# Performance work log

Measured on AMD Instinct MI355X. Metric: run time of the kernel, lower is better.

## Reference

```python
import jax, jax.numpy as jnp
import numpy as np

N_TOKEN = 100000
D = 1024  # d_embed == d_model == d_proj
CUTOFFS = [0, 20000, 60000, 100000]  # cutoff_ends
N_SEQ = 2048


def setup_inputs() -> dict:
    key = jax.random.key(0)
    ks = jax.random.split(key, 20)
    w = lambda k, s: jax.random.normal(k, s, dtype=jnp.float32) * 0.02
    return {
        "x": jax.random.randint(ks[0], (N_SEQ,), 0, N_TOKEN),
        "labels": jax.random.randint(ks[1], (N_SEQ,), 0, N_TOKEN),
        # adaptive embedding tables (d_emb_i = 1024 / 4**i) and projections [d_proj, d_emb_i]
        "emb_w0": w(ks[2], (20000, 1024)),
        "emb_w1": w(ks[3], (40000, 256)),
        "emb_w2": w(ks[4], (40000, 64)),
        "emb_proj0": w(ks[5], (1024, 1024)),
        "emb_proj1": w(ks[6], (1024, 256)),
        "emb_proj2": w(ks[7], (1024, 64)),
        # adaptive softmax output layers + projections
        "out_w0": w(ks[8], (20000, 1024)),
        "out_b0": jnp.zeros((20000,), jnp.float32),
        "out_w1": w(ks[9], (40000, 256)),
        "out_b1": jnp.zeros((40000,), jnp.float32),
        "out_w2": w(ks[10], (40000, 64)),
        "out_b2": jnp.zeros((40000,), jnp.float32),
        "out_proj0": w(ks[11], (1024, 1024)),
        "out_proj1": w(ks[12], (1024, 256)),
        "out_proj2": w(ks[13], (1024, 64)),
        # cluster head tokens (one per tail cluster)
        "cluster_w": w(ks[14], (2, 1024)),
        "cluster_b": jnp.zeros((2,), jnp.float32),
    }


def _forward(x, labels,
             emb_w0, emb_w1, emb_w2, emb_proj0, emb_proj1, emb_proj2,
             out_w0, out_b0, out_w1, out_b1, out_w2, out_b2,
             out_proj0, out_proj1, out_proj2, cluster_w, cluster_b):
    scale = jnp.asarray(D ** 0.5, jnp.float32)
    # AdaptiveEmbedding (div_val>1): per-cluster embed -> project to d_proj, scatter by range.
    # Equivalent vectorized form: build the full projected table once, then gather.
    table = jnp.concatenate([
        emb_w0 @ emb_proj0.T,   # [20000, D]
        emb_w1 @ emb_proj1.T,   # [40000, D]
        emb_w2 @ emb_proj2.T,   # [40000, D]
    ], axis=0)                   # [N_TOKEN, D]
    hidden = table[x] * scale    # [N, D]

    n = hidden.shape[0]
    rows = jnp.arange(n)

    # Head: cluster-0 vocab + one logit per tail cluster.
    head_w = jnp.concatenate([out_w0, cluster_w], axis=0)   # [20002, D]
    head_b = jnp.concatenate([out_b0, cluster_b], axis=0)   # [20002]
    head_logit = (hidden @ out_proj0) @ head_w.T + head_b   # [N, 20002]
    head_lp = jax.nn.log_softmax(head_logit, axis=-1)
    head_size = head_lp.shape[1]

    # Cluster 0: direct lookup in the head.
    lp0 = head_lp[rows, jnp.clip(labels, 0, CUTOFFS[1] - 1)]

    # Tail clusters: dense per-cluster log-softmax, gathered at shifted target,
    # plus the head cluster-token logprob (original TXL uses column -i).
    def tail(w, b, proj, i):
        l, r = CUTOFFS[i], CUTOFFS[i + 1]
        tail_lp = jax.nn.log_softmax((hidden @ proj) @ w.T + b, axis=-1)  # [N, r-l]
        t = jnp.clip(labels - l, 0, r - l - 1)
        return head_lp[:, head_size - i] + tail_lp[rows, t]

    lp1 = tail(out_w1, out_b1, out_proj1, 1)
    lp2 = tail(out_w2, out_b2, out_proj2, 2)

    logprob = jnp.where(labels < CUTOFFS[1], lp0,
               jnp.where(labels < CUTOFFS[2], lp1, lp2))
    return -logprob  # nll, [N]


def reference(x, labels,
              emb_w0, emb_w1, emb_w2, emb_proj0, emb_proj1, emb_proj2,
              out_w0, out_b0, out_w1, out_b1, out_w2, out_b2,
              out_proj0, out_proj1, out_proj2, cluster_w, cluster_b):
    return _forward(x, labels,
                    emb_w0, emb_w1, emb_w2, emb_proj0, emb_proj1, emb_proj2,
                    out_w0, out_b0, out_w1, out_b1, out_w2, out_b2,
                    out_proj0, out_proj1, out_proj2, cluster_w, cluster_b)
```

## Files before the change

kernel.cpp:

```cpp
#include <hip/hip_runtime.h>

typedef _Float16 f16x8 __attribute__((ext_vector_type(8)));
typedef _Float16 f16x4 __attribute__((ext_vector_type(4)));
typedef float f32x4 __attribute__((ext_vector_type(4)));
typedef unsigned char u8;

#define DEVI __device__ __forceinline__

constexpr int NROWS = 2048;
constexpr int HEADV = 20002;
constexpr int HEADP = 20480;
constexpr int NCBH  = 64;
constexpr int PSTH  = 64;
constexpr int VT    = 40000;
constexpr int VTP   = 40320;
constexpr int NCBT  = 126;
constexpr int PSTT  = 128;

DEVI void glds16(const void* g, void* l) {
  __builtin_amdgcn_global_load_lds((const __attribute__((address_space(1))) unsigned int*)g,
                                   (__attribute__((address_space(3))) unsigned int*)l,
                                   16, 0, 0);
}

#define VMW(N) asm volatile("s_waitcnt vmcnt(" #N ")" ::: "memory")
#define SCB    __builtin_amdgcn_sched_barrier(0)
#define BARR   __builtin_amdgcn_s_barrier()
#define PR1 __builtin_amdgcn_s_setprio(1)
#define PR0 __builtin_amdgcn_s_setprio(0)

#define SIG(r) (((r) >> 1) & 7)

DEVI unsigned int to_e4m3(float f) {
  unsigned u = __float_as_uint(f);
  unsigned s = (u >> 24) & 0x80u;
  float a = fabsf(f);
  if (!(a < 448.f)) return s | 0x7E;
  if (a < 0.00097656f) return s;
  int exp = (int)((u >> 23) & 0xFF) - 127;
  int qexp = exp < -6 ? -6 : exp;
  int n = __float2int_rn(a * exp2f((float)(3 - qexp)));
  if (n >= 16) { qexp++; n = 8; }
  return s | (unsigned)(n < 8 ? n : (((qexp + 7) << 3) | (n - 8)));
}

DEVI float fr8(unsigned b) {
  unsigned e = (b >> 3) & 15u, m = b & 7u;
  float v;
  if (e) v = __uint_as_float(((e + 120u) << 23) | (m << 20));
  else   v = (float)m * 0.001953125f;
  return (b & 0x80u) ? -v : v;
}

__global__ void prep_par(const int* __restrict__ x, const int* __restrict__ labels,
                         int* cl, int* headcol, int* tailpos, int* pos1, int* pos2,
                         int* L1, int* L2, int* T0, int* T1, int* T2, int* counts)
{
  int n = blockIdx.x * 256 + threadIdx.x;
  int l = labels[n];
  int c = l < 20000 ? 0 : (l < 60000 ? 1 : 2);
  cl[n] = c;
  headcol[n] = c == 0 ? l : (c == 1 ? 20001 : 20000);
  tailpos[n] = c == 1 ? l - 20000 : (c == 2 ? l - 60000 : 0);
  if (c == 1) { int s = atomicAdd(&counts[0], 1); pos1[n] = s; L1[s] = n; }
  else if (c == 2) { int s = atomicAdd(&counts[1], 1); pos2[n] = s; L2[s] = n; }
  int t = x[n];
  int tc = t < 20000 ? 0 : (t < 60000 ? 1 : 2);
  int s = atomicAdd(&counts[2 + tc], 1);
  (tc == 0 ? T0 : tc == 1 ? T1 : T2)[s] = n;
}

constexpr int PB_A = HEADP * 1024 / 8 / 256;
constexpr int PB_B = PB_A + VTP * 256 / 8 / 256;
constexpr int PB_C = PB_B + VTP * 128 / 8 / 256;
constexpr int PB_D = PB_C + 1024;
constexpr int PB_E = PB_D + 256;
constexpr int PB_F = PB_E + 64;
constexpr int PB_G = PB_F + 1024;
constexpr int PB_H = PB_G + 256;
constexpr int PB_I = PB_H + 128;

DEVI void cvt_f16(const float* src, _Float16* dst, int vb, int tid) {
  int g = vb * 256 + tid;
  float4 v = *(const float4*)(src + (size_t)g * 4);
  f16x4 o = {(_Float16)v.x, (_Float16)v.y, (_Float16)v.z, (_Float16)v.w};
  *(f16x4*)(dst + (size_t)g * 4) = o;
}

DEVI void tr32(const float* in, _Float16* out, int C, int bx, int by, int tid) {
  __shared__ float tile[32][33];
  int c0 = bx * 32, r0 = by * 32;
  int tx = tid & 31, ty = tid >> 5;
  for (int i = 0; i < 4; i++) {
    int c = c0 + tx; int r = r0 + ty + i * 8;
    tile[ty + i * 8][tx] = (c < C) ? in[(size_t)r * C + c] : 0.f;
  }
  __syncthreads();
  for (int i = 0; i < 4; i++)
    out[(size_t)(c0 + ty + i * 8) * 1024 + r0 + tx] = (_Float16)tile[tx][ty + i * 8];
}

DEVI unsigned long pack8(const float* v) {
  unsigned long p = 0;
  #pragma unroll
  for (int j = 0; j < 8; j++) p |= (unsigned long)to_e4m3(v[j] * 64.f) << (8 * j);
  return p;
}

__global__ void fused_pack(const float* __restrict__ out_w0, const float* __restrict__ out_b0,
                           const float* __restrict__ cluster_w, const float* __restrict__ cluster_b,
                           const float* __restrict__ out_w1, const float* __restrict__ out_b1,
                           const float* __restrict__ out_w2, const float* __restrict__ out_b2,
                           const float* __restrict__ emb_proj0, const float* __restrict__ emb_proj1,
                           const float* __restrict__ emb_proj2,
                           const float* __restrict__ out_proj0, const float* __restrict__ out_proj1,
                           const float* __restrict__ out_proj2,
                           u8* headw, float* headb,
                           u8* w1q, float* b1p, u8* w2q, float* b2p,
                           _Float16* ep0f, _Float16* ep1f, _Float16* ep2f,
                           _Float16* op0T, _Float16* op1T, _Float16* op2T,
                           int* lists, int* counts)
{
  int bid = blockIdx.x, tid = threadIdx.x;
  int zi = bid * 256 + tid;
  if (zi < 5 * 2048) lists[zi] = 0;
  if (bid == 41 && tid < 8) counts[tid] = 0;
  if (bid < PB_A) {
    int g = bid * 256 + tid;
    int r = g >> 7, sl = g & 127;
    float v[8] = {};
    if (r < 20000) {
      *(float4*)v = *(const float4*)(out_w0 + (size_t)r * 1024 + sl * 8);
      *(float4*)(v + 4) = *(const float4*)(out_w0 + (size_t)r * 1024 + sl * 8 + 4);
    } else if (r < 20002) {
      *(float4*)v = *(const float4*)(cluster_w + (size_t)(r - 20000) * 1024 + sl * 8);
      *(float4*)(v + 4) = *(const float4*)(cluster_w + (size_t)(r - 20000) * 1024 + sl * 8 + 4);
    }
    *(unsigned long*)(headw + (size_t)r * 1024 + ((sl ^ SIG(r)) << 3)) = pack8(v);
    if (g < HEADP) headb[g] = g < 20000 ? out_b0[g] : (g < HEADV ? cluster_b[g - 20000] : -1e30f);
  } else if (bid < PB_B) {
    int g = (bid - PB_A) * 256 + tid;
    int r = g >> 5, sl = g & 31;
    float v[8] = {};
    if (r < VT) {
      *(float4*)v = *(const float4*)(out_w1 + (size_t)r * 256 + sl * 8);
      *(float4*)(v + 4) = *(const float4*)(out_w1 + (size_t)r * 256 + sl * 8 + 4);
    }
    *(unsigned long*)(w1q + (size_t)r * 256 + ((sl ^ SIG(r)) << 3)) = pack8(v);
    if (g < VTP) b1p[g] = g < VT ? out_b1[g] : -1e30f;
  } else if (bid < PB_C) {
    int g = (bid - PB_B) * 256 + tid;
    int r = g >> 4, sl = g & 15;
    float v[8] = {};
    if (r < VT && sl < 8) {
      *(float4*)v = *(const float4*)(out_w2 + (size_t)r * 64 + sl * 8);
      *(float4*)(v + 4) = *(const float4*)(out_w2 + (size_t)r * 64 + sl * 8 + 4);
    }
    *(unsigned long*)(w2q + (size_t)r * 128 + ((sl ^ SIG(r)) << 3)) = pack8(v);
    if (g < VTP) b2p[g] = g < VT ? out_b2[g] : -1e30f;
  } else if (bid < PB_D) { cvt_f16(emb_proj0, ep0f, bid - PB_C, tid); }
  else if (bid < PB_E) { cvt_f16(emb_proj1, ep1f, bid - PB_D, tid); }
  else if (bid < PB_F) { cvt_f16(emb_proj2, ep2f, bid - PB_E, tid); }
  else if (bid < PB_G) { int l = bid - PB_F; tr32(out_proj0, op0T, 1024, l & 31, l >> 5, tid); }
  else if (bid < PB_H) { int l = bid - PB_G; tr32(out_proj1, op1T, 256, l & 7, l >> 3, tid); }
  else                 { int l = bid - PB_H; tr32(out_proj2, op2T, 64, l & 3, l >> 2, tid); }
}

DEVI void gat(const float* emb, const int* x, const int* list, _Float16* dst,
              int tbase, int vmax, int log2E, int vb, int tid) {
  int g = vb * 256 + tid;
  int r = g >> (log2E - 2);
  int e4 = (g & ((1 << (log2E - 2)) - 1)) << 2;
  int n = list[r];
  int tl = x[n] - tbase;
  tl = tl < 0 ? 0 : (tl >= vmax ? vmax - 1 : tl);
  float4 v = *(const float4*)(emb + ((size_t)tl << log2E) + e4);
  f16x4 o = {(_Float16)(v.x * 32.f), (_Float16)(v.y * 32.f),
             (_Float16)(v.z * 32.f), (_Float16)(v.w * 32.f)};
  *(f16x4*)(dst + ((size_t)r << log2E) + e4) = o;
}

__global__ void fused_gather(const float* __restrict__ emb_w0, const float* __restrict__ emb_w1,
                             const float* __restrict__ emb_w2, const int* __restrict__ x,
                             const int* __restrict__ T0, const int* __restrict__ T1,
                             const int* __restrict__ T2,
                             _Float16* E0, _Float16* E1, _Float16* E2)
{
  int bid = blockIdx.x, tid = threadIdx.x;
  if (bid < 2048)      gat(emb_w0, x, T0, E0, 0, 20000, 10, bid, tid);
  else if (bid < 2560) gat(emb_w1, x, T1, E1, 20000, 40000, 8, bid - 2048, tid);
  else                 gat(emb_w2, x, T2, E2, 60000, 40000, 6, bid - 2560, tid);
}

struct Seg128 {
  const _Float16* A; int lda;
  const _Float16* Wm; int ldw;
  _Float16* C; int ldc; int Nvalid;
  u8* Cq; int ldq;
  const int* amap; const int* cmap; const int* cnt;
  int K; int nblk;
};

DEVI void gemm128_body(const Seg128& s, int rb, int cb) {
  int valid = s.cnt ? *s.cnt : NROWS;
  if (rb * 128 >= valid) return;
  __shared__ __attribute__((aligned(16))) _Float16 As[128 * 32];
  __shared__ __attribute__((aligned(16))) _Float16 Ws[128 * 32];
  int tid = threadIdx.x;
  int lane = tid & 63, wid = tid >> 6;
  int wr = wid >> 1, wc = wid & 1;
  int sr = wid * 32 + (lane >> 2);
  int arow0 = rb * 128 + sr, arow1 = arow0 + 16;
  if (s.amap) { arow0 = s.amap[arow0]; arow1 = s.amap[arow1]; }
  int ko = (lane & 3) * 8;
  const _Float16* ag0 = s.A + (size_t)arow0 * s.lda + ko;
  const _Float16* ag1 = s.A + (size_t)arow1 * s.lda + ko;
  const _Float16* wg0 = s.Wm + (size_t)(cb * 128 + sr) * s.ldw + ko;
  const _Float16* wg1 = wg0 + (size_t)16 * s.ldw;
  _Float16* as0 = As + (wid * 32) * 32;
  _Float16* as1 = as0 + 16 * 32;
  _Float16* ws0 = Ws + (wid * 32) * 32;
  _Float16* ws1 = ws0 + 16 * 32;
  f32x4 acc[4][4] = {};
  int lr = lane & 15, lk = (lane >> 4) * 8;
  const int nk = s.K >> 5;
  for (int kt = 0; kt < nk; ++kt) {
    int kofs = kt * 32;
    glds16(ag0 + kofs, as0);
    glds16(ag1 + kofs, as1);
    glds16(wg0 + kofs, ws0);
    glds16(wg1 + kofs, ws1);
    __syncthreads();
    f16x8 af[4], bf[4];
    #pragma unroll
    for (int mi = 0; mi < 4; mi++)
      af[mi] = *(const f16x8*)(As + (wr * 64 + mi * 16 + lr) * 32 + lk);
    #pragma unroll
    for (int ni = 0; ni < 4; ni++)
      bf[ni] = *(const f16x8*)(Ws + (wc * 64 + ni * 16 + lr) * 32 + lk);
    #pragma unroll
    for (int mi = 0; mi < 4; mi++)
      #pragma unroll
      for (int ni = 0; ni < 4; ni++)
        acc[mi][ni] = __builtin_amdgcn_mfma_f32_16x16x32_f16(af[mi], bf[ni], acc[mi][ni], 0, 0, 0);
    __syncthreads();
  }
  #pragma unroll
  for (int mi = 0; mi < 4; mi++) {
    #pragma unroll
    for (int j = 0; j < 4; j++) {
      int rl = wr * 64 + mi * 16 + (lane >> 4) * 4 + j;
      int rg = rb * 128 + rl;
      if (rg >= valid) continue;
      int orow = s.cmap ? s.cmap[rg] : rg;
      #pragma unroll
      for (int ni = 0; ni < 4; ni++) {
        int col = cb * 128 + wc * 64 + ni * 16 + (lane & 15);
        if (col < s.Nvalid) {
          float v = acc[mi][ni][j];
          s.C[(size_t)orow * s.ldc + col] = (_Float16)v;
          if (s.Cq) {
            int sl = col >> 3;
            s.Cq[(size_t)orow * s.ldq + (((sl ^ SIG(orow)) << 3) | (col & 7))] = (u8)to_e4m3(v * 8.f);
          }
        }
      }
    }
  }
}

__global__ __launch_bounds__(256)
void gemm128_multi(Seg128 s0, Seg128 s1, Seg128 s2) {
  int b = blockIdx.x;
  if (b < s0.nblk)                    { gemm128_body(s0, b & 15, b >> 4); }
  else if (b < s0.nblk + s1.nblk)     { b -= s0.nblk; gemm128_body(s1, b & 15, b >> 4); }
  else                                { b -= s0.nblk + s1.nblk; gemm128_body(s2, b & 15, b >> 4); }
}

struct SegL {
  const u8* A; const u8* W; const float* bias; const int* cnt;
  float* pm; float* ps; int pstride; int K; int nrb; int nblk;
};

__global__ __launch_bounds__(512, 1)
void gemm_lse8_multi(SegL s0, SegL s1, SegL s2)
{
  constexpr int RSZ = 36864;
  __shared__ __attribute__((aligned(16))) u8 lds[3 * RSZ];

  int b = blockIdx.x;
  SegL s;
  if (b < s0.nblk) s = s0;
  else if (b < s0.nblk + s1.nblk) { s = s1; b -= s0.nblk; }
  else { s = s2; b -= s0.nblk + s1.nblk; }

  int q = s.nblk >> 3;
  int w = (b & 7) * q + (b >> 3);
  int rb = w % s.nrb, cb = w / s.nrb;
  int valid = s.cnt ? *s.cnt : NROWS;
  if (rb * 256 >= valid) return;

  const int K = s.K;
  int tid = threadIdx.x;
  int lane = tid & 63, wid = tid >> 6;
  int wm = wid >> 2, wn = wid & 3;
  int lr = lane & 15, g = lane >> 4;

  const u8* aS0 = s.A + (size_t)(rb * 256 + (tid >> 2)) * K + (tid & 3) * 16;
  const u8* aS1 = aS0 + (size_t)128 * K;
  const u8* bS0 = s.W + (size_t)((size_t)cb * 320 + (tid >> 2)) * K + (tid & 3) * 16;
  const u8* bS1 = bS0 + (size_t)128 * K;
  int t8 = tid & 255;
  const u8* bS2 = s.W + (size_t)((size_t)cb * 320 + 256 + (t8 >> 2)) * K + (t8 & 3) * 16;
  int dA0 = tid * 16, dA1 = dA0 + 8192;
  int dB0 = 16384 + tid * 16, dB1 = dB0 + 8192, dB2 = 32768 + t8 * 16;
  auto STAGE = [&](u8* rg, int k0) {
    glds16(aS0 + k0, rg + dA0);
    glds16(aS1 + k0, rg + dA1);
    glds16(bS0 + k0, rg + dB0);
    glds16(bS1 + k0, rg + dB1);
    glds16(bS2 + k0, rg + dB2);
  };

  int sig = (lr >> 1) & 7;
  int aro = (wm * 128 + lr) * 64;
  int bro = 16384 + (wn * 80 + lr) * 64;
  int ks0 = (g ^ sig) * 8;
  int ks1 = ((4 + g) ^ sig) * 8;

  f32x4 acc[8][5] = {};
  const int nk = K >> 6;

  asm volatile("s_waitcnt vmcnt(0) lgkmcnt(0)" ::: "memory");
  STAGE(lds, 0);
  STAGE(lds + RSZ, (nk > 1 ? 1 : 0) * 64);
  VMW(5); SCB; BARR; SCB;

  for (int t = 0; t < nk; ++t) {
    int ts = (t + 2 > nk - 1) ? nk - 1 : t + 2;
    STAGE(lds + ((t + 2) % 3) * RSZ, ts * 64);
    const u8* cur = lds + (t % 3) * RSZ;
    PR1;
    #pragma unroll
    for (int kk = 0; kk < 2; ++kk) {
      int ko = kk ? ks1 : ks0;
      long bq[5];
      #pragma unroll
      for (int ni = 0; ni < 5; ++ni) bq[ni] = *(const long*)(cur + bro + ni * 1024 + ko);
      #pragma unroll
      for (int mi = 0; mi < 8; ++mi) {
        long av = *(const long*)(cur + aro + mi * 1024 + ko);
        #pragma unroll
        for (int ni = 0; ni < 5; ++ni)
          acc[mi][ni] = __builtin_amdgcn_mfma_f32_16x16x32_fp8_fp8(av, bq[ni], acc[mi][ni], 0, 0, 0);
      }
    }
    PR0;
    VMW(5); SCB; BARR; SCB;
  }
  VMW(0); SCB; BARR; SCB;

  float* lm = (float*)lds;
  float* lsm = lm + 1024;
  float bv[5];
  #pragma unroll
  for (int ni = 0; ni < 5; ++ni) bv[ni] = s.bias[cb * 320 + wn * 80 + ni * 16 + lr];
  constexpr float INV = 1.f / 512.f;
  #pragma unroll
  for (int mi = 0; mi < 8; ++mi) {
    #pragma unroll
    for (int j = 0; j < 4; ++j) {
      float v0 = acc[mi][0][j] * INV + bv[0];
      float v1 = acc[mi][1][j] * INV + bv[1];
      float v2 = acc[mi][2][j] * INV + bv[2];
      float v3 = acc[mi][3][j] * INV + bv[3];
      float v4 = acc[mi][4][j] * INV + bv[4];
      float m = fmaxf(fmaxf(fmaxf(v0, v1), fmaxf(v2, v3)), v4);
      #pragma unroll
      for (int d = 1; d < 16; d <<= 1) m = fmaxf(m, __shfl_xor(m, d));
      float sm = __expf(v0 - m) + __expf(v1 - m) + __expf(v2 - m) + __expf(v3 - m) + __expf(v4 - m);
      #pragma unroll
      for (int d = 1; d < 16; d <<= 1) sm += __shfl_xor(sm, d);
      if (lr == 0) {
        int row = wm * 128 + mi * 16 + g * 4 + j;
        lm[wn * 256 + row] = m; lsm[wn * 256 + row] = sm;
      }
    }
  }
  __syncthreads();
  if (tid < 256) {
    float m0 = lm[tid], m1 = lm[256 + tid], m2 = lm[512 + tid], m3 = lm[768 + tid];
    float M = fmaxf(fmaxf(m0, m1), fmaxf(m2, m3));
    float S = lsm[tid] * __expf(m0 - M) + lsm[256 + tid] * __expf(m1 - M)
            + lsm[512 + tid] * __expf(m2 - M) + lsm[768 + tid] * __expf(m3 - M);
    int gr = rb * 256 + tid;
    s.pm[(size_t)gr * s.pstride + cb] = M;
    s.ps[(size_t)gr * s.pstride + cb] = S;
  }
}

DEVI float lsew(const float* m, const float* s, int nb, int lane) {
  float M = -3e38f;
  for (int i = lane; i < nb; i += 64) M = fmaxf(M, m[i]);
  #pragma unroll
  for (int d = 1; d < 64; d <<= 1) M = fmaxf(M, __shfl_xor(M, d));
  float S = 0.f;
  for (int i = lane; i < nb; i += 64) S += s[i] * __expf(m[i] - M);
  #pragma unroll
  for (int d = 1; d < 64; d <<= 1) S += __shfl_xor(S, d);
  return M + __logf(S);
}

__global__ void finish_kernel(const _Float16* __restrict__ ph0, const u8* __restrict__ headw,
                              const float* __restrict__ headb,
                              const _Float16* __restrict__ ph1c, const u8* __restrict__ w1q,
                              const float* __restrict__ b1p,
                              const _Float16* __restrict__ ph2c, const u8* __restrict__ w2q,
                              const float* __restrict__ b2p,
                              const int* __restrict__ headcol, const int* __restrict__ tailpos,
                              const int* __restrict__ pos1, const int* __restrict__ pos2,
                              const int* __restrict__ cl,
                              const float* __restrict__ pmh, const float* __restrict__ psh,
                              const float* __restrict__ pm1, const float* __restrict__ ps1,
                              const float* __restrict__ pm2, const float* __restrict__ ps2,
                              float* __restrict__ out)
{
  int n = blockIdx.x;
  int tid = threadIdx.x, lane = tid & 63, wid = tid >> 6;
  __shared__ float sh[6];
  int c = cl[n];
  constexpr float IW = 1.f / 64.f;
  if (wid == 0) {
    int hc = headcol[n];
    const f16x8* a = (const f16x8*)(ph0 + (size_t)n * 1024 + lane * 16);
    float s = 0.f;
    #pragma unroll
    for (int u = 0; u < 2; u++) {
      int sl = lane * 2 + u;
      unsigned long wq = *(const unsigned long*)(headw + (size_t)hc * 1024 + (((sl ^ SIG(hc)) << 3)));
      f16x8 av = a[u];
      #pragma unroll
      for (int j = 0; j < 8; j++) s += (float)av[j] * fr8((unsigned)(wq >> (8 * j)) & 0xFFu);
    }
    #pragma unroll
    for (int d = 1; d < 64; d <<= 1) s += __shfl_xor(s, d);
    if (lane == 0) sh[0] = s * IW + headb[hc];
  } else if (wid == 1 && c == 1) {
    int p = pos1[n], t = tailpos[n];
    f16x4 av = *(const f16x4*)(ph1c + (size_t)p * 256 + lane * 4);
    int sl = lane >> 1;
    const u8* ww = w1q + (size_t)t * 256 + ((sl ^ SIG(t)) << 3) + (lane & 1) * 4;
    float s = (float)av[0] * fr8(ww[0]) + (float)av[1] * fr8(ww[1])
            + (float)av[2] * fr8(ww[2]) + (float)av[3] * fr8(ww[3]);
    #pragma unroll
    for (int d = 1; d < 64; d <<= 1) s += __shfl_xor(s, d);
    float l = lsew(pm1 + (size_t)p * PSTT, ps1 + (size_t)p * PSTT, NCBT, lane);
    if (lane == 0) { sh[1] = s * IW + b1p[t]; sh[4] = l; }
  } else if (wid == 2 && c == 2) {
    int p = pos2[n], t = tailpos[n];
    const _Float16* a = ph2c + (size_t)p * 128 + lane * 2;
    int sl = lane >> 2;
    const u8* ww = w2q + (size_t)t * 128 + ((sl ^ SIG(t)) << 3) + (lane & 3) * 2;
    float s = (float)a[0] * fr8(ww[0]) + (float)a[1] * fr8(ww[1]);
    #pragma unroll
    for (int d = 1; d < 64; d <<= 1) s += __shfl_xor(s, d);
    float l = lsew(pm2 + (size_t)p * PSTT, ps2 + (size_t)p * PSTT, NCBT, lane);
    if (lane == 0) { sh[2] = s * IW + b2p[t]; sh[5] = l; }
  } else if (wid == 3) {
    float l = lsew(pmh + (size_t)n * PSTH, psh + (size_t)n * PSTH, NCBH, lane);
    if (lane == 0) sh[3] = l;
  }
  __syncthreads();
  if (tid == 0) {
    float nll = sh[3] - sh[0];
    if (c == 1)      nll += sh[4] - sh[1];
    else if (c == 2) nll += sh[5] - sh[2];
    out[n] = nll;
  }
}

extern "C" void kernel_launch(void* const* d_in, const int* in_sizes, int n_in,
                              void* d_out, int out_size, void* d_ws, size_t ws_size,
                              hipStream_t stream)
{
  const int*   x         = (const int*)d_in[0];
  const int*   labels    = (const int*)d_in[1];
  const float* emb_w0    = (const float*)d_in[2];
  const float* emb_w1    = (const float*)d_in[3];
  const float* emb_w2    = (const float*)d_in[4];
  const float* emb_proj0 = (const float*)d_in[5];
  const float* emb_proj1 = (const float*)d_in[6];
  const float* emb_proj2 = (const float*)d_in[7];
  const float* out_w0    = (const float*)d_in[8];
  const float* out_b0    = (const float*)d_in[9];
  const float* out_w1    = (const float*)d_in[10];
  const float* out_b1    = (const float*)d_in[11];
  const float* out_w2    = (const float*)d_in[12];
  const float* out_b2    = (const float*)d_in[13];
  const float* out_proj0 = (const float*)d_in[14];
  const float* out_proj1 = (const float*)d_in[15];
  const float* out_proj2 = (const float*)d_in[16];
  const float* cluster_w = (const float*)d_in[17];
  const float* cluster_b = (const float*)d_in[18];
  float* out = (float*)d_out;

  char* ws = (char*)d_ws;
  size_t off = 0;
  auto alloc = [&](size_t bytes) -> void* {
    void* p = ws + off;
    off = (off + bytes + 255) & ~(size_t)255;
    return p;
  };
  u8*    headw = (u8*)alloc((size_t)HEADP * 1024);
  float* headb = (float*)alloc((size_t)HEADP * 4);
  u8*    w1q   = (u8*)alloc((size_t)VTP * 256);
  float* b1p   = (float*)alloc((size_t)VTP * 4);
  u8*    w2q   = (u8*)alloc((size_t)VTP * 128);
  float* b2p   = (float*)alloc((size_t)VTP * 4);
  _Float16* ep0f = (_Float16*)alloc((size_t)1024 * 1024 * 2);
  _Float16* ep1f = (_Float16*)alloc((size_t)1024 * 256 * 2);
  _Float16* ep2f = (_Float16*)alloc((size_t)1024 * 64 * 2);
  _Float16* op0T = (_Float16*)alloc((size_t)1024 * 1024 * 2);
  _Float16* op1T = (_Float16*)alloc((size_t)256 * 1024 * 2);
  _Float16* op2T = (_Float16*)alloc((size_t)128 * 1024 * 2);
  _Float16* E0   = (_Float16*)alloc((size_t)NROWS * 1024 * 2);
  _Float16* E1   = (_Float16*)alloc((size_t)NROWS * 256 * 2);
  _Float16* E2   = (_Float16*)alloc((size_t)NROWS * 64 * 2);
  _Float16* hid  = (_Float16*)alloc((size_t)NROWS * 1024 * 2);
  _Float16* ph0  = (_Float16*)alloc((size_t)NROWS * 1024 * 2);
  u8*       ph0q = (u8*)alloc((size_t)NROWS * 1024);
  _Float16* ph1c = (_Float16*)alloc((size_t)NROWS * 256 * 2);
  u8*       ph1q = (u8*)alloc((size_t)NROWS * 256);
  _Float16* ph2c = (_Float16*)alloc((size_t)NROWS * 128 * 2);
  u8*       ph2q = (u8*)alloc((size_t)NROWS * 128);
  float* pmh = (float*)alloc((size_t)NROWS * PSTH * 4);
  float* psh = (float*)alloc((size_t)NROWS * PSTH * 4);
  float* pm1 = (float*)alloc((size_t)NROWS * PSTT * 4);
  float* ps1 = (float*)alloc((size_t)NROWS * PSTT * 4);
  float* pm2 = (float*)alloc((size_t)NROWS * PSTT * 4);
  float* ps2 = (float*)alloc((size_t)NROWS * PSTT * 4);
  int* lists = (int*)alloc(5 * NROWS * 4);
  int* L1 = lists;
  int* L2 = lists + 2048;
  int* T0 = lists + 4096;
  int* T1 = lists + 6144;
  int* T2 = lists + 8192;
  int* counts  = (int*)alloc(16 * 4);
  int* cl      = (int*)alloc(NROWS * 4);
  int* headcol = (int*)alloc(NROWS * 4);
  int* tailpos = (int*)alloc(NROWS * 4);
  int* pos1    = (int*)alloc(NROWS * 4);
  int* pos2    = (int*)alloc(NROWS * 4);
  (void)ws_size; (void)in_sizes; (void)n_in; (void)out_size;

  fused_pack<<<PB_I, 256, 0, stream>>>(out_w0, out_b0, cluster_w, cluster_b,
                                       out_w1, out_b1, out_w2, out_b2,
                                       emb_proj0, emb_proj1, emb_proj2,
                                       out_proj0, out_proj1, out_proj2,
                                       headw, headb, w1q, b1p, w2q, b2p,
                                       ep0f, ep1f, ep2f, op0T, op1T, op2T,
                                       lists, counts);

  prep_par<<<8, 256, 0, stream>>>(x, labels, cl, headcol, tailpos, pos1, pos2,
                                  L1, L2, T0, T1, T2, counts);

  fused_gather<<<2688, 256, 0, stream>>>(emb_w0, emb_w1, emb_w2, x, T0, T1, T2, E0, E1, E2);

  Seg128 h0 = {E0, 1024, ep0f, 1024, hid, 1024, 1024, nullptr, 0, nullptr, T0, counts + 2, 1024, 128};
  Seg128 h1 = {E1, 256,  ep1f, 256,  hid, 1024, 1024, nullptr, 0, nullptr, T1, counts + 3, 256,  128};
  Seg128 h2 = {E2, 64,   ep2f, 64,   hid, 1024, 1024, nullptr, 0, nullptr, T2, counts + 4, 64,   128};
  gemm128_multi<<<384, 256, 0, stream>>>(h0, h1, h2);

  Seg128 p0 = {hid, 1024, op0T, 1024, ph0,  1024, 1024, ph0q, 1024, nullptr, nullptr, nullptr,   1024, 128};
  Seg128 p1 = {hid, 1024, op1T, 1024, ph1c, 256,  256,  ph1q, 256,  L1,      nullptr, counts + 0, 1024, 32};
  Seg128 p2 = {hid, 1024, op2T, 1024, ph2c, 128,  128,  ph2q, 128,  L2,      nullptr, counts + 1, 1024, 16};
  gemm128_multi<<<176, 256, 0, stream>>>(p0, p1, p2);

  SegL l0 = {ph0q, headw, headb, nullptr,    pmh, psh, PSTH, 1024, 8, 8 * NCBH};
  SegL l1 = {ph1q, w1q,   b1p,   counts + 0, pm1, ps1, PSTT, 256,  8, 8 * NCBT};
  SegL l2 = {ph2q, w2q,   b2p,   counts + 1, pm2, ps2, PSTT, 128,  8, 8 * NCBT};
  gemm_lse8_multi<<<8 * NCBH + 16 * NCBT, 512, 0, stream>>>(l0, l1, l2);

  finish_kernel<<<NROWS, 256, 0, stream>>>(ph0, headw, headb, ph1c, w1q, b1p,
                                           ph2c, w2q, b2p, headcol, tailpos, pos1, pos2, cl,
                                           pmh, psh, pm1, ps1, pm2, ps2, out);
}
```

Before: 297.3 us.

## Switch fp8 logits GEMM to 32x32x64 scaled MFMA with 4x2 wave layout

Replaces the 16x16x32 fp8 MFMA tiling (8x5 tiles per wave, 2x4 wave grid) with the gfx950 32x32x64 scaled f8f6f4 MFMA (2x5 tiles per wave, 4x2 wave grid). This cuts the number of MFMA issues and LDS fragment reads per K-step and reuses each B fragment across two A tiles. The epilogue's row mapping and cross-lane reductions are reworked for the 32-wide output layout, and the cross-wave merge now combines two column partials instead of four. The swizzled LDS offsets are recomputed for 32-row fragments, so a bank-conflict pattern change or a wrong lane mapping is the main risk.

```diff
diff --git a/kernel.cpp b/kernel.cpp
--- a/kernel.cpp
+++ b/kernel.cpp
@@ -3,6 +3,8 @@
 typedef _Float16 f16x8 __attribute__((ext_vector_type(8)));
 typedef _Float16 f16x4 __attribute__((ext_vector_type(4)));
 typedef float f32x4 __attribute__((ext_vector_type(4)));
+typedef float f32x16 __attribute__((ext_vector_type(16)));
+typedef int i32x8 __attribute__((ext_vector_type(8)));
 typedef unsigned char u8;
 
 #define DEVI __device__ __forceinline__
@@ -303,8 +305,8 @@
   const int K = s.K;
   int tid = threadIdx.x;
   int lane = tid & 63, wid = tid >> 6;
-  int wm = wid >> 2, wn = wid & 3;
-  int lr = lane & 15, g = lane >> 4;
+  int wm = wid >> 1, wn = wid & 1;
+  int l31 = lane & 31;
 
   const u8* aS0 = s.A + (size_t)(rb * 256 + (tid >> 2)) * K + (tid & 3) * 16;
   const u8* aS1 = aS0 + (size_t)128 * K;
@@ -322,13 +324,16 @@
     glds16(bS2 + k0, rg + dB2);
   };
 
-  int sig = (lr >> 1) & 7;
-  int aro = (wm * 128 + lr) * 64;
-  int bro = 16384 + (wn * 80 + lr) * 64;
-  int ks0 = (g ^ sig) * 8;
-  int ks1 = ((4 + g) ^ sig) * 8;
-
-  f32x4 acc[8][5] = {};
+  int sig = (l31 >> 1) & 7;
+  int hb = (lane >> 5) * 4;
+  int o0 = ((hb + 0) ^ sig) << 3;
+  int o1 = ((hb + 1) ^ sig) << 3;
+  int o2 = ((hb + 2) ^ sig) << 3;
+  int o3 = ((hb + 3) ^ sig) << 3;
+  int aro = (wm * 64 + l31) * 64;
+  int bro = 16384 + (wn * 160 + l31) * 64;
+
+  f32x16 acc[2][5] = {};
   const int nk = K >> 6;
 
   asm volatile("s_waitcnt vmcnt(0) lgkmcnt(0)" ::: "memory");
@@ -336,24 +341,33 @@
   STAGE(lds + RSZ, (nk > 1 ? 1 : 0) * 64);
   VMW(5); SCB; BARR; SCB;
 
+  union UV { i32x8 v; long l[4]; };
   for (int t = 0; t < nk; ++t) {
     int ts = (t + 2 > nk - 1) ? nk - 1 : t + 2;
     STAGE(lds + ((t + 2) % 3) * RSZ, ts * 64);
     const u8* cur = lds + (t % 3) * RSZ;
     PR1;
-    #pragma unroll
-    for (int kk = 0; kk < 2; ++kk) {
-      int ko = kk ? ks1 : ks0;
-      long bq[5];
-      #pragma unroll
-      for (int ni = 0; ni < 5; ++ni) bq[ni] = *(const long*)(cur + bro + ni * 1024 + ko);
-      #pragma unroll
-      for (int mi = 0; mi < 8; ++mi) {
-        long av = *(const long*)(cur + aro + mi * 1024 + ko);
-        #pragma unroll
-        for (int ni = 0; ni < 5; ++ni)
-          acc[mi][ni] = __builtin_amdgcn_mfma_f32_16x16x32_fp8_fp8(av, bq[ni], acc[mi][ni], 0, 0, 0);
-      }
+    UV a0, a1;
+    a0.l[0] = *(const long*)(cur + aro + o0);
+    a0.l[1] = *(const long*)(cur + aro + o1);
+    a0.l[2] = *(const long*)(cur + aro + o2);
+    a0.l[3] = *(const long*)(cur + aro + o3);
+    a1.l[0] = *(const long*)(cur + aro + 2048 + o0);
+    a1.l[1] = *(const long*)(cur + aro + 2048 + o1);
+    a1.l[2] = *(const long*)(cur + aro + 2048 + o2);
+    a1.l[3] = *(const long*)(cur + aro + 2048 + o3);
+    #pragma unroll
+    for (int ni = 0; ni < 5; ++ni) {
+      UV bv;
+      const u8* bp = cur + bro + ni * 2048;
+      bv.l[0] = *(const long*)(bp + o0);
+      bv.l[1] = *(const long*)(bp + o1);
+      bv.l[2] = *(const long*)(bp + o2);
+      bv.l[3] = *(const long*)(bp + o3);
+      acc[0][ni] = __builtin_amdgcn_mfma_scale_f32_32x32x64_f8f6f4(
+                     a0.v, bv.v, acc[0][ni], 0, 0, 0, 127, 0, 127);
+      acc[1][ni] = __builtin_amdgcn_mfma_scale_f32_32x32x64_f8f6f4(
+                     a1.v, bv.v, acc[1][ni], 0, 0, 0, 127, 0, 127);
     }
     PR0;
     VMW(5); SCB; BARR; SCB;
@@ -361,38 +375,38 @@
   VMW(0); SCB; BARR; SCB;
 
   float* lm = (float*)lds;
-  float* lsm = lm + 1024;
-  float bv[5];
+  float* lsm = lm + 512;
+  float bv5[5];
   #pragma unroll
-  for (int ni = 0; ni < 5; ++ni) bv[ni] = s.bias[cb * 320 + wn * 80 + ni * 16 + lr];
+  for (int ni = 0; ni < 5; ++ni) bv5[ni] = s.bias[cb * 320 + wn * 160 + ni * 32 + l31];
   constexpr float INV = 1.f / 512.f;
+  int rl4 = 4 * (lane >> 5);
   #pragma unroll
-  for (int mi = 0; mi < 8; ++mi) {
-    #pragma unroll
-    for (int j = 0; j < 4; ++j) {
-      float v0 = acc[mi][0][j] * INV + bv[0];
-      float v1 = acc[mi][1][j] * INV + bv[1];
-      float v2 = acc[mi][2][j] * INV + bv[2];
-      float v3 = acc[mi][3][j] * INV + bv[3];
-      float v4 = acc[mi][4][j] * INV + bv[4];
+  for (int mi = 0; mi < 2; ++mi) {
+    #pragma unroll
+    for (int r = 0; r < 16; ++r) {
+      float v0 = acc[mi][0][r] * INV + bv5[0];
+      float v1 = acc[mi][1][r] * INV + bv5[1];
+      float v2 = acc[mi][2][r] * INV + bv5[2];
+      float v3 = acc[mi][3][r] * INV + bv5[3];
+      float v4 = acc[mi][4][r] * INV + bv5[4];
       float m = fmaxf(fmaxf(fmaxf(v0, v1), fmaxf(v2, v3)), v4);
       #pragma unroll
-      for (int d = 1; d < 16; d <<= 1) m = fmaxf(m, __shfl_xor(m, d));
+      for (int d = 1; d < 32; d <<= 1) m = fmaxf(m, __shfl_xor(m, d));
       float sm = __expf(v0 - m) + __expf(v1 - m) + __expf(v2 - m) + __expf(v3 - m) + __expf(v4 - m);
       #pragma unroll
-      for (int d = 1; d < 16; d <<= 1) sm += __shfl_xor(sm, d);
-      if (lr == 0) {
-        int row = wm * 128 + mi * 16 + g * 4 + j;
+      for (int d = 1; d < 32; d <<= 1) sm += __shfl_xor(sm, d);
+      if (l31 == 0) {
+        int row = wm * 64 + mi * 32 + (r & 3) + 8 * (r >> 2) + rl4;
         lm[wn * 256 + row] = m; lsm[wn * 256 + row] = sm;
       }
     }
   }
   __syncthreads();
   if (tid < 256) {
-    float m0 = lm[tid], m1 = lm[256 + tid], m2 = lm[512 + tid], m3 = lm[768 + tid];
-    float M = fmaxf(fmaxf(m0, m1), fmaxf(m2, m3));
-    float S = lsm[tid] * __expf(m0 - M) + lsm[256 + tid] * __expf(m1 - M)
-            + lsm[512 + tid] * __expf(m2 - M) + lsm[768 + tid] * __expf(m3 - M);
+    float m0 = lm[tid], m1 = lm[256 + tid];
+    float M = fmaxf(m0, m1);
+    float S = lsm[tid] * __expf(m0 - M) + lsm[256 + tid] * __expf(m1 - M);
     int gr = rb * 256 + tid;
     s.pm[(size_t)gr * s.pstride + cb] = M;
     s.ps[(size_t)gr * s.pstride + cb] = S;
```

After: 286.1 us. 3.8% less time.
